# Kernel optimization log

Measured on AMD Instinct MI355X. Metric: run time of the kernel, lower is better.

## Reference

```python
import jax, jax.numpy as jnp
import numpy as np

ENTITY_TYPES = ['PER', 'ORG', 'LOC', 'MISC', 'GPE', 'DATE', 'TIME', 'MONEY', 'PERCENT',
                'FAC', 'EVENT', 'LAW', 'LANGUAGE', 'NORP', 'ORDINAL', 'CARDINAL', 'PRODUCT', 'QUANTITY']
TAGS = ['<PAD>', 'O'] + [f'{p}-{t}' for t in ENTITY_TYPES for p in ('B', 'I')]
TAG2IDX = {t: i for i, t in enumerate(TAGS)}
PAD_IDX = TAG2IDX['<PAD>']
O_IDX = TAG2IDX['O']
LAMBDA_MISS = 1.2
LAMBDA_FP = 1.0
LAMBDA_TRANSITION = 0.8
EPS = 1e-8


def _split_tag(tag):
    if tag in {'O', '<PAD>'} or '-' not in tag:
        return (tag, None)
    prefix, label = tag.split('-', 1)
    return (prefix, label)


def build_valid_transition_mask():
    n = len(TAGS)
    valid = np.zeros((n, n), dtype=np.float32)
    for prev_idx, prev_tag in enumerate(TAGS):
        prev_prefix, prev_label = _split_tag(prev_tag)
        for curr_idx, curr_tag in enumerate(TAGS):
            curr_prefix, curr_label = _split_tag(curr_tag)
            if curr_tag == '<PAD>' or curr_tag == 'O' or curr_prefix == 'B':
                ok = True
            elif curr_prefix == 'I':
                ok = (prev_prefix in {'B', 'I'}) and (prev_label == curr_label)
            else:
                ok = False
            valid[prev_idx, curr_idx] = 1.0 if ok else 0.0
    return valid


def setup_inputs() -> dict:
    key = jax.random.key(0)
    k1, k2 = jax.random.split(key)
    B, T, C = 128, 4096, len(TAGS)  # C = 38
    logits = jax.random.normal(k1, (B, T, C), dtype=jnp.float32)
    labels = jax.random.randint(k2, (B, T), 0, C, dtype=jnp.int32)
    valid_transition_mask = jnp.asarray(build_valid_transition_mask())  # [C, C]
    return {'logits': logits, 'labels': labels, 'valid_transition_mask': valid_transition_mask}


def _masked_mean(x, mask):
    # mean of x over positions where mask is True (0 if mask empty)
    cnt = jnp.sum(mask)
    return jnp.sum(jnp.where(mask, x, 0.0)) / jnp.maximum(cnt, 1).astype(x.dtype)


def reference(logits, labels, valid_transition_mask):
    # logits: [B, T, C]; labels: [B, T] int; valid_transition_mask: [C, C]
    logp = jax.nn.log_softmax(logits, axis=-1)            # [B, T, C]
    probs = jnp.exp(logp)                                  # softmax(logits)

    valid = labels != PAD_IDX                              # [B, T]
    # cross entropy with ignore_index=PAD (unweighted mean over valid tokens)
    gold_logp = jnp.take_along_axis(logp, labels[..., None], axis=-1)[..., 0]
    ce_loss = _masked_mean(-gold_logp, valid)

    p_o = probs[..., O_IDX]                                # [B, T]
    gold_entity = valid & (labels != O_IDX)
    gold_o = valid & (labels == O_IDX)

    # miss penalty: -log(1 - p_o) on gold entity tokens
    miss_penalty = _masked_mean(-jnp.log(jnp.clip(1.0 - p_o, EPS)), gold_entity)
    # false-positive penalty: -log(1 - (1 - p_o)) = -log(p_o) on gold O tokens
    fp_penalty = _masked_mean(-jnp.log(jnp.clip(p_o, EPS)), gold_o)

    # transition penalty: sum of prev_probs (outer) curr_probs over invalid (prev,curr)
    # pairs. Algebraically: prev . (invalid @ curr) per position, avoids [B,T,C,C].
    invalid = 1.0 - valid_transition_mask                  # [C, C]
    invalid_mass = jnp.einsum('btc,cd,btd->bt', probs[:, :-1, :], invalid, probs[:, 1:, :])
    tmask = valid[:, 1:] & valid[:, :-1]
    transition_penalty = _masked_mean(invalid_mass, tmask)

    return (ce_loss + LAMBDA_MISS * miss_penalty + LAMBDA_FP * fp_penalty
            + LAMBDA_TRANSITION * transition_penalty)
```

## Files before the change

kernel.cpp:

```cpp
#include <hip/hip_runtime.h>


#define NCLS 38
#define SLF 2440

__global__ __launch_bounds__(256, 4) void ner_main(const float* __restrict__ logits,
                                                   const int* __restrict__ labels,
                                                   float* __restrict__ partials) {
    __shared__ float S[4][SLF];

    const int tid  = threadIdx.x;
    const int lane = tid & 63;
    const int wv   = tid >> 6;
    const int W    = blockIdx.x * 4 + wv;
    const int row  = (int)(((unsigned)W * 64528u) >> 22);
    const int wrow = W - row * 65;
    const long long tok0 = (long long)row * 4096 + 63 * wrow;
    const long long tok  = tok0 + lane;

    float* sl = S[wv];

    const int l = labels[tok];
    {
        const long long basef = tok0 * NCLS;
        const int off = (int)(basef & 3);
        const float4* g4 = reinterpret_cast<const float4*>(logits + (basef - off));
        const int nf4 = 608 + (off ? 1 : 0);
#pragma unroll
        for (int i = 0; i < 10; ++i) {
            const int idx = lane + i * 64;
            if (idx < nf4)
                __builtin_amdgcn_global_load_lds(
                    (const __attribute__((address_space(1))) void*)(g4 + idx),
                    (__attribute__((address_space(3))) void*)(sl + i * 256),
                    16, 0, 0);
        }
        asm volatile("s_waitcnt vmcnt(0)" ::: "memory");
        sl += off;
    }

    float v[NCLS];
    {
        const float2* lp = reinterpret_cast<const float2*>(sl + lane * NCLS);
        float2* vv = reinterpret_cast<float2*>(v);
#pragma unroll
        for (int i = 0; i < NCLS / 2; ++i) vv[i] = lp[i];
    }
    const float gold = sl[lane * NCLS + l];

    float s = 0.f;
#pragma unroll
    for (int c = 0; c < NCLS; ++c) { const float e = __expf(v[c]); v[c] = e; s += e; }
    const float inv = 1.f / s;
    const float lg  = __logf(s);

    float ce_s = 0.f, mi_s = 0.f, fp_s = 0.f, tr_s = 0.f, cnt = 0.f;

    const bool own_tok = (lane < 63) || (wrow == 64);
    if (own_tok && l != 0) {
        ce_s = lg - gold; cnt += 1.f;
        const float po = v[1] * inv;
        if (l == 1) { fp_s = -__logf(fmaxf(po,       1e-8f)); cnt += 256.f; }
        else        { mi_s = -__logf(fmaxf(1.f - po, 1e-8f)); }
    }

    const int   lnext = __shfl_down(l, 1, 64);
    const float qinv  = __shfl_down(inv, 1, 64);
    float qv[18];
#pragma unroll
    for (int j = 0; j < 18; ++j) qv[j] = __shfl_down(v[3 + 2 * j], 1, 64);

    if (lane < 63 && l != 0 && lnext != 0) {
        float m = 0.f;
#pragma unroll
        for (int j = 0; j < 18; ++j)
            m += qv[j] * (s - v[2 + 2 * j] - v[3 + 2 * j]);
        tr_s = m * inv * qinv; cnt += 65536.f;
    }

    float vals[5] = {ce_s, mi_s, fp_s, tr_s, cnt};
#pragma unroll
    for (int k = 0; k < 5; ++k) {
        float x = vals[k];
#pragma unroll
        for (int o = 32; o >= 1; o >>= 1) x += __shfl_down(x, o, 64);
        vals[k] = x;
    }
    if (lane == 0) {
        *reinterpret_cast<float4*>(partials + W * 8) =
            make_float4(vals[0], vals[1], vals[2], vals[3]);
        partials[W * 8 + 4] = vals[4];
    }
}

__global__ __launch_bounds__(1024) void ner_reduce(const float* __restrict__ partials,
                                                   float* __restrict__ out, int nwaves) {
    __shared__ float acc[7];
    const int tid = threadIdx.x;
    if (tid < 7) acc[tid] = 0.f;
    __syncthreads();
    float s_ce = 0.f, s_mi = 0.f, s_fp = 0.f, s_tr = 0.f;
    float c_ce = 0.f, c_fp = 0.f, c_tr = 0.f;
    for (int i = tid; i < nwaves; i += 1024) {
        const float4 p = *reinterpret_cast<const float4*>(partials + i * 8);
        const float pc = partials[i * 8 + 4];
        s_ce += p.x; s_mi += p.y; s_fp += p.z; s_tr += p.w;
        const float tc = floorf(pc * (1.f / 65536.f));
        const float rem = pc - tc * 65536.f;
        const float fc = floorf(rem * (1.f / 256.f));
        c_tr += tc; c_fp += fc; c_ce += rem - fc * 256.f;
    }
    float vals[7] = {s_ce, s_mi, s_fp, s_tr, c_ce, c_fp, c_tr};
#pragma unroll
    for (int k = 0; k < 7; ++k) {
        float x = vals[k];
#pragma unroll
        for (int o = 32; o >= 1; o >>= 1) x += __shfl_down(x, o, 64);
        if ((tid & 63) == 0) atomicAdd(&acc[k], x);
    }
    __syncthreads();
    if (tid == 0) {
        const float ce_c = acc[4], fp_c = acc[5], tr_c = acc[6];
        const float mi_c = ce_c - fp_c;
        const float ce = acc[0] / fmaxf(ce_c, 1.f);
        const float mi = acc[1] / fmaxf(mi_c, 1.f);
        const float fp = acc[2] / fmaxf(fp_c, 1.f);
        const float tr = acc[3] / fmaxf(tr_c, 1.f);
        out[0] = ce + 1.2f * mi + 1.0f * fp + 0.8f * tr;
    }
}

extern "C" void kernel_launch(void* const* d_in, const int* in_sizes, int n_in,
                              void* d_out, int out_size, void* d_ws, size_t ws_size,
                              hipStream_t stream) {
    const float* logits = (const float*)d_in[0];
    const int*   labels = (const int*)d_in[1];
    float* partials = (float*)d_ws;

    const long long N = (long long)in_sizes[1];
    const int rows   = (int)(N / 4096);
    const int nwaves = rows * 65;
    const int nblk   = nwaves / 4;

    hipLaunchKernelGGL(ner_main, dim3(nblk), dim3(256), 0, stream, logits, labels, partials);
    hipLaunchKernelGGL(ner_reduce, dim3(1), dim3(1024), 0, stream, partials, (float*)d_out, nwaves);
}
```

Before: 117.8 us.

## Make waves persistent over several tiles with double-buffered async LDS loads

Each wave now walks 4-5 tiles of 63 tokens, with 2048 waves in place of one wave per tile. It double-buffers the global-to-LDS loads so the next tile's fetch overlaps the current tile's compute, with partial vmcnt waits. Counts are packed differently: the transition count gets its own slot because a per-wave count would overflow the old packed encoding. Fewer waves means fewer partials and less launch overhead, but also less parallelism for hiding latency on a bandwidth-bound read of about 80MB.

```diff
diff --git a/kernel.cpp b/kernel.cpp
--- a/kernel.cpp
+++ b/kernel.cpp
@@ -2,94 +2,112 @@
 
 
 #define NCLS 38
-#define SLF 2440
+#define BUFF 2440
 
-__global__ __launch_bounds__(256, 4) void ner_main(const float* __restrict__ logits,
+__global__ __launch_bounds__(128, 4) void ner_main(const float* __restrict__ logits,
                                                    const int* __restrict__ labels,
-                                                   float* __restrict__ partials) {
-    __shared__ float S[4][SLF];
+                                                   float* __restrict__ partials,
+                                                   int ntiles) {
+    __shared__ float S[2][2][BUFF];
 
     const int tid  = threadIdx.x;
     const int lane = tid & 63;
     const int wv   = tid >> 6;
-    const int W    = blockIdx.x * 4 + wv;
-    const int row  = (int)(((unsigned)W * 64528u) >> 22);
-    const int wrow = W - row * 65;
-    const long long tok0 = (long long)row * 4096 + 63 * wrow;
-    const long long tok  = tok0 + lane;
+    const int gw   = blockIdx.x * 2 + wv;
+    const int nt   = 4 + (gw < (ntiles - 8192));
 
-    float* sl = S[wv];
+    long long tok0[5]; int offv[5], wrow[5], lab[5];
+#pragma unroll
+    for (int t = 0; t < 5; ++t) {
+        const int tile = gw + 2048 * t;
+        const int row  = (int)(((unsigned)tile * 64528u) >> 22);
+        wrow[t] = tile - row * 65;
+        tok0[t] = (long long)row * 4096 + 63 * wrow[t];
+        offv[t] = ((int)tok0[t] & 1) * 2;
+        lab[t]  = (t < nt) ? labels[tok0[t] + lane] : 0;
+    }
 
-    const int l = labels[tok];
-    {
-        const long long basef = tok0 * NCLS;
-        const int off = (int)(basef & 3);
-        const float4* g4 = reinterpret_cast<const float4*>(logits + (basef - off));
-        const int nf4 = 608 + (off ? 1 : 0);
+    auto issue = [&](int t) {
+        const float4* g4 = reinterpret_cast<const float4*>(logits + tok0[t] * NCLS - offv[t]);
+        float* dst = &S[wv][t & 1][0];
+        const int nf4 = 608 + (offv[t] ? 1 : 0);
 #pragma unroll
         for (int i = 0; i < 10; ++i) {
             const int idx = lane + i * 64;
             if (idx < nf4)
                 __builtin_amdgcn_global_load_lds(
                     (const __attribute__((address_space(1))) void*)(g4 + idx),
-                    (__attribute__((address_space(3))) void*)(sl + i * 256),
+                    (__attribute__((address_space(3))) void*)(dst + i * 256),
                     16, 0, 0);
         }
-        asm volatile("s_waitcnt vmcnt(0)" ::: "memory");
-        sl += off;
+    };
+
+    issue(0);
+
+    float ce_s = 0.f, mi_s = 0.f, fp_s = 0.f, tr_s = 0.f, c_cefp = 0.f, c_tr = 0.f;
+
+#pragma unroll
+    for (int t = 0; t < 5; ++t) {
+        if (t >= nt) break;
+        const bool more = (t + 1 < nt);
+        if (more) issue(t + 1);
+        if (more) asm volatile("s_waitcnt vmcnt(10)" ::: "memory");
+        else      asm volatile("s_waitcnt vmcnt(0)"  ::: "memory");
+
+        const float* sl = &S[wv][t & 1][offv[t]];
+        const int l = lab[t];
+
+        float v[NCLS];
+        {
+            const float2* lp = reinterpret_cast<const float2*>(sl + lane * NCLS);
+            float2* vv = reinterpret_cast<float2*>(v);
+#pragma unroll
+            for (int i = 0; i < NCLS / 2; ++i) vv[i] = lp[i];
+        }
+        const float gold = sl[lane * NCLS + l];
+
+        float s = 0.f;
+#pragma unroll
+        for (int c = 0; c < NCLS; ++c) { const float e = __expf(v[c]); v[c] = e; s += e; }
+        const float inv = 1.f / s;
+        const float lg  = __logf(s);
+
+        const bool own = (lane < 63) || (wrow[t] == 64);
+        if (own && l != 0) {
+            ce_s += lg - gold; c_cefp += 1.f;
+            const float po = v[1] * inv;
+            if (l == 1) { fp_s -= __logf(fmaxf(po,       1e-8f)); c_cefp += 1024.f; }
+            else        { mi_s -= __logf(fmaxf(1.f - po, 1e-8f)); }
+        }
+
+        const int   lnext = __shfl_down(l, 1, 64);
+        const float qinv  = __shfl_down(inv, 1, 64);
+        float qv[18];
+#pragma unroll
+        for (int j = 0; j < 18; ++j) qv[j] = __shfl_down(v[3 + 2 * j], 1, 64);
+
+        if (lane < 63 && l != 0 && lnext != 0) {
+            float m = 0.f;
+#pragma unroll
+            for (int j = 0; j < 18; ++j)
+                m += qv[j] * (s - v[2 + 2 * j] - v[3 + 2 * j]);
+            tr_s += m * inv * qinv; c_tr += 1.f;
+        }
     }
 
-    float v[NCLS];
-    {
-        const float2* lp = reinterpret_cast<const float2*>(sl + lane * NCLS);
-        float2* vv = reinterpret_cast<float2*>(v);
+    float vals[6] = {ce_s, mi_s, fp_s, tr_s, c_cefp, c_tr};
 #pragma unroll
-        for (int i = 0; i < NCLS / 2; ++i) vv[i] = lp[i];
-    }
-    const float gold = sl[lane * NCLS + l];
-
-    float s = 0.f;
-#pragma unroll
-    for (int c = 0; c < NCLS; ++c) { const float e = __expf(v[c]); v[c] = e; s += e; }
-    const float inv = 1.f / s;
-    const float lg  = __logf(s);
-
-    float ce_s = 0.f, mi_s = 0.f, fp_s = 0.f, tr_s = 0.f, cnt = 0.f;
-
-    const bool own_tok = (lane < 63) || (wrow == 64);
-    if (own_tok && l != 0) {
-        ce_s = lg - gold; cnt += 1.f;
-        const float po = v[1] * inv;
-        if (l == 1) { fp_s = -__logf(fmaxf(po,       1e-8f)); cnt += 256.f; }
-        else        { mi_s = -__logf(fmaxf(1.f - po, 1e-8f)); }
-    }
-
-    const int   lnext = __shfl_down(l, 1, 64);
-    const float qinv  = __shfl_down(inv, 1, 64);
-    float qv[18];
-#pragma unroll
-    for (int j = 0; j < 18; ++j) qv[j] = __shfl_down(v[3 + 2 * j], 1, 64);
-
-    if (lane < 63 && l != 0 && lnext != 0) {
-        float m = 0.f;
-#pragma unroll
-        for (int j = 0; j < 18; ++j)
-            m += qv[j] * (s - v[2 + 2 * j] - v[3 + 2 * j]);
-        tr_s = m * inv * qinv; cnt += 65536.f;
-    }
-
-    float vals[5] = {ce_s, mi_s, fp_s, tr_s, cnt};
-#pragma unroll
-    for (int k = 0; k < 5; ++k) {
+    for (int k = 0; k < 6; ++k) {
         float x = vals[k];
 #pragma unroll
         for (int o = 32; o >= 1; o >>= 1) x += __shfl_down(x, o, 64);
         vals[k] = x;
     }
     if (lane == 0) {
-        *reinterpret_cast<float4*>(partials + W * 8) =
+        *reinterpret_cast<float4*>(partials + gw * 8) =
             make_float4(vals[0], vals[1], vals[2], vals[3]);
-        partials[W * 8 + 4] = vals[4];
+        *reinterpret_cast<float2*>(partials + gw * 8 + 4) =
+            make_float2(vals[4], vals[5]);
     }
 }
 
@@ -103,12 +121,10 @@
     float c_ce = 0.f, c_fp = 0.f, c_tr = 0.f;
     for (int i = tid; i < nwaves; i += 1024) {
         const float4 p = *reinterpret_cast<const float4*>(partials + i * 8);
-        const float pc = partials[i * 8 + 4];
+        const float2 q = *reinterpret_cast<const float2*>(partials + i * 8 + 4);
         s_ce += p.x; s_mi += p.y; s_fp += p.z; s_tr += p.w;
-        const float tc = floorf(pc * (1.f / 65536.f));
-        const float rem = pc - tc * 65536.f;
-        const float fc = floorf(rem * (1.f / 256.f));
-        c_tr += tc; c_fp += fc; c_ce += rem - fc * 256.f;
+        const float fc = floorf(q.x * (1.f / 1024.f));
+        c_fp += fc; c_ce += q.x - fc * 1024.f; c_tr += q.y;
     }
     float vals[7] = {s_ce, s_mi, s_fp, s_tr, c_ce, c_fp, c_tr};
 #pragma unroll
@@ -122,11 +138,8 @@
     if (tid == 0) {
         const float ce_c = acc[4], fp_c = acc[5], tr_c = acc[6];
         const float mi_c = ce_c - fp_c;
-        const float ce = acc[0] / fmaxf(ce_c, 1.f);
-        const float mi = acc[1] / fmaxf(mi_c, 1.f);
-        const float fp = acc[2] / fmaxf(fp_c, 1.f);
-        const float tr = acc[3] / fmaxf(tr_c, 1.f);
-        out[0] = ce + 1.2f * mi + 1.0f * fp + 0.8f * tr;
+        out[0] = acc[0] / fmaxf(ce_c, 1.f) + 1.2f * (acc[1] / fmaxf(mi_c, 1.f))
+               + 1.0f * (acc[2] / fmaxf(fp_c, 1.f)) + 0.8f * (acc[3] / fmaxf(tr_c, 1.f));
     }
 }
 
@@ -139,9 +152,12 @@
 
     const long long N = (long long)in_sizes[1];
     const int rows   = (int)(N / 4096);
-    const int nwaves = rows * 65;
-    const int nblk   = nwaves / 4;
+    const int ntiles = rows * 65;
+    const int nwaves = 2048;
+    const int nblk   = nwaves / 2;
 
-    hipLaunchKernelGGL(ner_main, dim3(nblk), dim3(256), 0, stream, logits, labels, partials);
-    hipLaunchKernelGGL(ner_reduce, dim3(1), dim3(1024), 0, stream, partials, (float*)d_out, nwaves);
+    hipLaunchKernelGGL(ner_main, dim3(nblk), dim3(128), 0, stream,
+                       logits, labels, partials, ntiles);
+    hipLaunchKernelGGL(ner_reduce, dim3(1), dim3(1024), 0, stream,
+                       partials, (float*)d_out, nwaves);
 }
```

After: 117.8 us. Within noise of the previous version (-0.0%).
